# Performance work log

Hardware: AMD Instinct MI355X
Metric: run time of the kernel (lower is better)

## Reference

```python
import jax, jax.numpy as jnp
import numpy as np

B, P, M, C = 8192, 8, 2048, 1024


def setup_inputs() -> dict:
    key = jax.random.key(0)
    k1, k2 = jax.random.split(key)
    stdv = 1.0 / np.sqrt(C)
    inp = jax.random.normal(k1, (B, C), dtype=jnp.float32)
    weight = jax.random.uniform(k2, (P, M, C), dtype=jnp.float32, minval=-stdv, maxval=stdv)
    return {"input": inp, "weight": weight}


def reference(input, weight):
    # scores: [B, P, M] = <input_c, weight_pmc>
    att = jnp.einsum('bc,pmc->bpm', input, weight)
    att = jax.nn.softmax(att, axis=2)
    # combine with the same memory bank as values: [B, P, C]
    out = jnp.einsum('bpm,pmc->bpc', att, weight)
    return out
```

## Files before the change

### kernel.cpp

```cpp
#include <hip/hip_runtime.h>
#include <hip/hip_bf16.h>
#include <cstdint>
#include <cstddef>

#define B_SZ 8192
#define P_SZ 8
#define M_SZ 2048
#define C_SZ 1024

using bfrag = __attribute__((ext_vector_type(8))) short;
using facc  = __attribute__((ext_vector_type(4))) float;
using u16x4 = __attribute__((ext_vector_type(4))) unsigned short;

typedef __attribute__((address_space(1))) const void g_void;
typedef __attribute__((address_space(3))) void l_void;

__device__ __forceinline__ unsigned short f2bf(float x) {
    union { __hip_bfloat16 h; unsigned short u; } cv;
    cv.h = __float2bfloat16(x);
    return cv.u;
}
__device__ __forceinline__ float bf2f(unsigned short u) {
    union { unsigned int i; float f; } cv;
    cv.i = ((unsigned int)u) << 16;
    return cv.f;
}

#define S_BARRIER()     asm volatile("s_barrier" ::: "memory")
#define LGKM0_BARRIER() asm volatile("s_waitcnt lgkmcnt(0)\n\ts_barrier" ::: "memory")
#define WAIT_VM(n)      asm volatile("s_waitcnt vmcnt(" #n ")" ::: "memory")
#define BAR() asm volatile("s_waitcnt lgkmcnt(0)\n\ts_barrier" ::: "memory")
#define WAIT_VM8() asm volatile("s_waitcnt vmcnt(8)" ::: "memory")

__global__ void cvt_q_kernel(const float* __restrict__ in, unsigned short* __restrict__ q) {
    const size_t i = (size_t)blockIdx.x * blockDim.x + threadIdx.x;
    const float4 v = ((const float4*)in)[i];
    u16x4 o = { f2bf(v.x), f2bf(v.y), f2bf(v.z), f2bf(v.w) };
    ((u16x4*)q)[i] = o;
}

__global__ void cvt_w_kernel(const float* __restrict__ w,
                             unsigned short* __restrict__ wb,
                             unsigned short* __restrict__ wt) {
    __shared__ float t[32][33];
    const int bid = blockIdx.x;
    const int p  = bid >> 11;
    const int m0 = ((bid >> 5) & 63) << 5;
    const int c0 = (bid & 31) << 5;
    const int tx = threadIdx.x & 7;
    const int ty = threadIdx.x >> 3;
    const float4 v = *(const float4*)(w + ((size_t)p*M_SZ + m0 + ty)*C_SZ + c0 + tx*4);
    u16x4 o = { f2bf(v.x), f2bf(v.y), f2bf(v.z), f2bf(v.w) };
    *(u16x4*)(wb + ((size_t)p*M_SZ + m0 + ty)*C_SZ + c0 + tx*4) = o;
    t[ty][tx*4+0] = v.x; t[ty][tx*4+1] = v.y; t[ty][tx*4+2] = v.z; t[ty][tx*4+3] = v.w;
    __syncthreads();
    float4 u2;
    u2.x = t[tx*4+0][ty]; u2.y = t[tx*4+1][ty]; u2.z = t[tx*4+2][ty]; u2.w = t[tx*4+3][ty];
    u16x4 o2 = { f2bf(u2.x), f2bf(u2.y), f2bf(u2.z), f2bf(u2.w) };
    *(u16x4*)(wt + ((size_t)p*C_SZ + c0 + ty)*M_SZ + m0 + tx*4) = o2;
}

template<int KLEN, int NTN, int CPX, int MODE>
__global__ __launch_bounds__(256, 2)
void gemm_tile(const unsigned short* __restrict__ A,
               const unsigned short* __restrict__ Bm,
               unsigned short* __restrict__ Pout,
               float* __restrict__ Oout,
               int p)
{
    __shared__ alignas(16) char lds[32768];
    const int tid  = threadIdx.x;
    const int lane = tid & 63;
    const int wid  = tid >> 6;
    const int wr   = wid >> 1;
    const int wc   = wid & 1;
    const int g    = lane >> 4;
    const int l15  = lane & 15;

    const int logical = (blockIdx.x & 7) * CPX + (blockIdx.x >> 3);
    const int mt = logical / NTN;
    const int nt = logical % NTN;

    const unsigned short* Abase = A  + (size_t)mt * 128 * KLEN;
    const unsigned short* Bbase = Bm + (size_t)nt * 128 * KLEN;

    facc acc[4][4];
    #pragma unroll
    for (int i = 0; i < 4; ++i)
        #pragma unroll
        for (int j = 0; j < 4; ++j) acc[i][j] = facc{0.f, 0.f, 0.f, 0.f};
    float rs[4] = {0.f, 0.f, 0.f, 0.f};

    constexpr int NKT = KLEN / 32;

    auto stage = [&](int kt) {
        char* buf = lds + (kt & 1) * 16384;
        const unsigned short* As = Abase + kt * 32;
        const unsigned short* Bs = Bbase + kt * 32;
        #pragma unroll
        for (int i = 0; i < 2; ++i) {
            const int o  = i * 4096 + tid * 16;
            const int r  = o >> 6;
            const int s  = (o >> 4) & 3;
            const int cs = s ^ ((r >> 1) & 3);
            __builtin_amdgcn_global_load_lds((g_void*)(As + (size_t)r * KLEN + cs * 8),
                                             (l_void*)(buf + i * 4096 + ((tid >> 6) << 10)),
                                             16, 0, 0);
        }
        #pragma unroll
        for (int i = 0; i < 2; ++i) {
            const int o  = i * 4096 + tid * 16;
            const int r  = o >> 6;
            const int s  = (o >> 4) & 3;
            const int cs = s ^ ((r >> 1) & 3);
            __builtin_amdgcn_global_load_lds((g_void*)(Bs + (size_t)r * KLEN + cs * 8),
                                             (l_void*)(buf + 8192 + i * 4096 + ((tid >> 6) << 10)),
                                             16, 0, 0);
        }
    };

    stage(0);
    stage(1);

    const int cb = ((((l15 >> 1) & 3) ^ g) << 4);

    for (int kt = 0; kt < NKT; ++kt) {
        if (kt + 1 < NKT) { WAIT_VM(4); } else { WAIT_VM(0); }
        S_BARRIER();
        const char* Ab = lds + (kt & 1) * 16384;
        const char* Bb = Ab + 8192;
        bfrag af[4], bb[4];
        #pragma unroll
        for (int mf = 0; mf < 4; ++mf)
            af[mf] = *(const bfrag*)(Ab + (wr * 64 + mf * 16 + l15) * 64 + cb);
        #pragma unroll
        for (int nf = 0; nf < 4; ++nf)
            bb[nf] = *(const bfrag*)(Bb + (wc * 64 + nf * 16 + l15) * 64 + cb);
        LGKM0_BARRIER();
        if (kt + 2 < NKT) stage(kt + 2);
        if (MODE == 1) {
            #pragma unroll
            for (int mf = 0; mf < 4; ++mf)
                #pragma unroll
                for (int e = 0; e < 8; ++e)
                    rs[mf] += bf2f((unsigned short)af[mf][e]);
        }
        #pragma unroll
        for (int mf = 0; mf < 4; ++mf)
            #pragma unroll
            for (int nf = 0; nf < 4; ++nf)
                acc[mf][nf] = __builtin_amdgcn_mfma_f32_16x16x32_bf16(af[mf], bb[nf], acc[mf][nf], 0, 0, 0);
    }

    if (MODE == 0) {
        const int prow0 = mt * 128 + wr * 64;
        const int pcol0 = nt * 128 + wc * 64;
        #pragma unroll
        for (int mf = 0; mf < 4; ++mf)
            #pragma unroll
            for (int j = 0; j < 4; ++j) {
                const size_t rbase = (size_t)(prow0 + mf * 16 + g * 4 + j) * M_SZ + pcol0 + l15;
                #pragma unroll
                for (int nf = 0; nf < 4; ++nf)
                    Pout[rbase + nf * 16] = f2bf(__expf(acc[mf][nf][j]));
            }
    } else {
        const int orow0 = mt * 128 + wr * 64;
        const int ocol0 = nt * 128 + wc * 64;
        #pragma unroll
        for (int mf = 0; mf < 4; ++mf) {
            float d = rs[mf];
            d += __shfl_xor(d, 16);
            d += __shfl_xor(d, 32);
            #pragma unroll
            for (int j = 0; j < 4; ++j) {
                const float inv = 1.0f / __shfl(d, g * 4 + j);
                const size_t rbase = ((size_t)(orow0 + mf * 16 + g * 4 + j) * P_SZ + p) * C_SZ
                                   + ocol0 + l15;
                #pragma unroll
                for (int nf = 0; nf < 4; ++nf)
                    Oout[rbase + nf * 16] = acc[mf][nf][j] * inv;
            }
        }
    }
}

constexpr int NTHREADS = 512;
constexpr int BR = 64;
constexpr int MT = 32;
constexpr int NT = M_SZ / MT;

constexpr int WS_OFF   = 0;
constexpr int WST_OFF  = 65536;
constexpr int SRED_OFF = 131072;
constexpr int PS_OFF   = 158720;
constexpr int DEN_OFF  = 162816;
constexpr int LDS_BYTES = 163328;

__device__ __forceinline__ void stage_ws(const unsigned short* wsrcTile, char* ldsWs, int tid) {
    #pragma unroll
    for (int k = 0; k < 8; ++k) {
        const int o = k*8192 + tid*16;
        const int m = o >> 11;
        const int s = (o & 2047) >> 4;
        const unsigned short* src = wsrcTile + (size_t)m*C_SZ + ((s ^ (m & 7)) << 3);
        char* dst = ldsWs + k*8192 + ((tid >> 6) << 10);
        __builtin_amdgcn_global_load_lds((g_void*)src, (l_void*)dst, 16, 0, 0);
    }
}

__device__ __forceinline__ void stage_wst(const unsigned short* wtsrcTile, char* ldsWsT, int tid) {
    #pragma unroll
    for (int k = 0; k < 8; ++k) {
        const int o = k*8192 + tid*16;
        const int c  = o >> 6;
        const int mh = (o & 63) >> 4;
        const unsigned short* src = wtsrcTile + (size_t)c*M_SZ + mh*8;
        char* dst = ldsWsT + k*8192 + ((tid >> 6) << 10);
        __builtin_amdgcn_global_load_lds((g_void*)src, (l_void*)dst, 16, 0, 0);
    }
}

__global__ __launch_bounds__(NTHREADS, 2)
void emu_main(const unsigned short* __restrict__ qB,
              const unsigned short* __restrict__ wB,
              const unsigned short* __restrict__ wtB,
              float* __restrict__ out)
{
    extern __shared__ char lds[];
    const int tid  = threadIdx.x;
    const int lane = tid & 63;
    const int wid  = tid >> 6;
    const int rh   = wid >> 2;
    const int kq   = wid & 3;
    const int g    = lane >> 4;
    const int l15  = lane & 15;

    const int p    = blockIdx.x & 7;
    const int row0 = (blockIdx.x >> 3) * BR;

    const unsigned short* wbp = wB  + (size_t)p * M_SZ * C_SZ;
    const unsigned short* wtp = wtB + (size_t)p * C_SZ * M_SZ;

    bfrag qreg[2][8];
    #pragma unroll
    for (int rf = 0; rf < 2; ++rf) {
        const int qrow = row0 + (rh*2 + rf)*16 + l15;
        const unsigned short* qp = qB + (size_t)qrow*C_SZ + kq*256 + g*8;
        #pragma unroll
        for (int kc = 0; kc < 8; ++kc)
            qreg[rf][kc] = *(const bfrag*)(qp + kc*32);
    }

    facc acc[2][16];
    #pragma unroll
    for (int i = 0; i < 2; ++i)
        #pragma unroll
        for (int j = 0; j < 16; ++j) acc[i][j] = facc{0.f,0.f,0.f,0.f};
    float dsum[4] = {0.f, 0.f, 0.f, 0.f};

    const int fid    = rh*4 + kq;
    const int rf_own = rh*2 + (kq >> 1);
    const int mf_own = kq & 1;

    stage_ws (wbp, lds + WS_OFF,  tid);
    stage_wst(wtp, lds + WST_OFF, tid);

    for (int mt = 0; mt < NT; ++mt) {
        const int mtn = (mt + 1 < NT) ? (mt + 1) : (NT - 1);

        WAIT_VM8();
        BAR();

        facc sacc[2][2];
        #pragma unroll
        for (int i = 0; i < 2; ++i) { sacc[i][0] = facc{0,0,0,0}; sacc[i][1] = facc{0,0,0,0}; }
        {
            const char* wsr0 = lds + WS_OFF + l15*2048;
            const char* wsr1 = wsr0 + 32768;
            const int xr = l15 & 7;
            #pragma unroll
            for (int kc = 0; kc < 8; ++kc) {
                const int slog = kq*32 + kc*4 + g;
                const int off  = (slog ^ xr) << 4;
                bfrag b0 = *(const bfrag*)(wsr0 + off);
                bfrag b1 = *(const bfrag*)(wsr1 + off);
                #pragma unroll
                for (int rf = 0; rf < 2; ++rf) {
                    sacc[rf][0] = __builtin_amdgcn_mfma_f32_16x16x32_bf16(qreg[rf][kc], b0, sacc[rf][0], 0, 0, 0);
                    sacc[rf][1] = __builtin_amdgcn_mfma_f32_16x16x32_bf16(qreg[rf][kc], b1, sacc[rf][1], 0, 0, 0);
                }
            }
        }

        #pragma unroll
        for (int j2 = 0; j2 < 4; ++j2) {
            if (j2 != kq) {
                const int s = kq - (kq > j2 ? 1 : 0);
                float* dstp = (float*)(lds + SRED_OFF) + ((rh*4 + j2)*3 + s)*288;
                #pragma unroll
                for (int j = 0; j < 4; ++j)
                    dstp[(g*4 + j)*18 + l15] = sacc[j2 >> 1][j2 & 1][j];
            }
        }
        BAR();

        stage_ws(wbp + (size_t)mtn*MT*C_SZ, lds + WS_OFF, tid);

        {
            facc own = (kq == 0) ? sacc[0][0] : (kq == 1) ? sacc[0][1]
                     : (kq == 2) ? sacc[1][0] : sacc[1][1];
            const float* srcp = (const float*)(lds + SRED_OFF) + fid*3*288;
            float ps[4];
            #pragma unroll
            for (int j = 0; j < 4; ++j) {
                const int e = (g*4 + j)*18 + l15;
                float v = own[j] + srcp[e] + srcp[288 + e] + srcp[576 + e];
                ps[j] = __expf(v);
                dsum[j] += ps[j];
            }
            #pragma unroll
            for (int j = 0; j < 4; ++j)
                *(unsigned short*)(lds + PS_OFF + ((rf_own*16 + g*4 + j)*32 + mf_own*16 + l15)*2)
                    = f2bf(ps[j]);
        }

        WAIT_VM8();
        BAR();

        {
            bfrag pa0 = *(const bfrag*)(lds + PS_OFF + ((rh*2 + 0)*16 + l15)*64 + g*16);
            bfrag pa1 = *(const bfrag*)(lds + PS_OFF + ((rh*2 + 1)*16 + l15)*64 + g*16);
            const char* wtb = lds + WST_OFF + (kq*256 + l15)*64 + g*16;
            #pragma unroll
            for (int cf = 0; cf < 16; ++cf) {
                bfrag bw = *(const bfrag*)(wtb + cf*1024);
                acc[0][cf] = __builtin_amdgcn_mfma_f32_16x16x32_bf16(pa0, bw, acc[0][cf], 0, 0, 0);
                acc[1][cf] = __builtin_amdgcn_mfma_f32_16x16x32_bf16(pa1, bw, acc[1][cf], 0, 0, 0);
            }
        }
        BAR();

        stage_wst(wtp + (size_t)mtn*MT, lds + WST_OFF, tid);
    }

    #pragma unroll
    for (int j = 0; j < 4; ++j) {
        float v = dsum[j];
        v += __shfl_xor(v, 1); v += __shfl_xor(v, 2);
        v += __shfl_xor(v, 4); v += __shfl_xor(v, 8);
        if (l15 == 0) ((float*)(lds + DEN_OFF))[fid*16 + g*4 + j] = v;
    }
    BAR();

    const float* denp = (const float*)(lds + DEN_OFF);
    #pragma unroll
    for (int rf = 0; rf < 2; ++rf) {
        const int rfg = rh*2 + rf;
        #pragma unroll
        for (int j = 0; j < 4; ++j) {
            const int rr = g*4 + j;
            const float inv = 1.0f / (denp[(rfg*2 + 0)*16 + rr] + denp[(rfg*2 + 1)*16 + rr]);
            const size_t b = (size_t)row0 + rfg*16 + rr;
            float* op = out + (b*P_SZ + p)*C_SZ + kq*256 + l15;
            #pragma unroll
            for (int cf = 0; cf < 16; ++cf)
                op[cf*16] = acc[rf][cf][j] * inv;
        }
    }
}

__global__ void emu_fallback(const float* __restrict__ inF, const float* __restrict__ wF,
                             float* __restrict__ out)
{
    __shared__ float sc[M_SZ];
    __shared__ float qs[C_SZ];
    __shared__ float wsum[4];
    const int b = blockIdx.x;
    const int tid = threadIdx.x;
    for (int c = tid; c < C_SZ; c += 256) qs[c] = inF[(size_t)b*C_SZ + c];
    __syncthreads();
    for (int p = 0; p < P_SZ; ++p) {
        const float* wp = wF + (size_t)p*M_SZ*C_SZ;
        for (int m = tid; m < M_SZ; m += 256) {
            float d = 0.f;
            const float* wr = wp + (size_t)m*C_SZ;
            for (int c = 0; c < C_SZ; ++c) d += qs[c]*wr[c];
            sc[m] = __expf(d);
        }
        __syncthreads();
        float part = 0.f;
        for (int m = tid; m < M_SZ; m += 256) part += sc[m];
        #pragma unroll
        for (int sft = 1; sft < 64; sft <<= 1) part += __shfl_xor(part, sft);
        if ((tid & 63) == 0) wsum[tid >> 6] = part;
        __syncthreads();
        const float rin = 1.0f / (wsum[0] + wsum[1] + wsum[2] + wsum[3]);
        float o0=0,o1=0,o2=0,o3=0;
        for (int m = 0; m < M_SZ; ++m) {
            const float pm = sc[m];
            const float4 w4 = *(const float4*)(wp + (size_t)m*C_SZ + tid*4);
            o0 += pm*w4.x; o1 += pm*w4.y; o2 += pm*w4.z; o3 += pm*w4.w;
        }
        float* op = out + ((size_t)b*P_SZ + p)*C_SZ + tid*4;
        op[0]=o0*rin; op[1]=o1*rin; op[2]=o2*rin; op[3]=o3*rin;
        __syncthreads();
    }
}

extern "C" void kernel_launch(void* const* d_in, const int* in_sizes, int n_in,
                              void* d_out, int out_size, void* d_ws, size_t ws_size,
                              hipStream_t stream)
{
    (void)in_sizes; (void)n_in; (void)out_size;
    const float* inF = (const float*)d_in[0];
    const float* wF  = (const float*)d_in[1];
    float* out = (float*)d_out;

    const size_t wbE = (size_t)P_SZ * M_SZ * C_SZ;
    const size_t qE  = (size_t)B_SZ * C_SZ;
    const size_t pME = (size_t)B_SZ * M_SZ;
    const size_t needFull  = (wbE*2 + qE + pME) * sizeof(unsigned short);
    const size_t needFused = (wbE*2 + qE) * sizeof(unsigned short);

    if (ws_size >= needFull) {
        unsigned short* wb = (unsigned short*)d_ws;
        unsigned short* wt = wb + wbE;
        unsigned short* qb = wt + wbE;
        unsigned short* Pb = qb + qE;
        cvt_q_kernel<<<(unsigned)(qE/4/256), 256, 0, stream>>>(inF, qb);
        cvt_w_kernel<<<P_SZ*64*32, 256, 0, stream>>>(wF, wb, wt);
        for (int p = 0; p < P_SZ; ++p) {
            gemm_tile<C_SZ, 16, 128, 0><<<1024, 256, 0, stream>>>(
                qb, wb + (size_t)p*M_SZ*C_SZ, Pb, nullptr, p);
            gemm_tile<M_SZ, 8, 64, 1><<<512, 256, 0, stream>>>(
                Pb, wt + (size_t)p*C_SZ*M_SZ, nullptr, out, p);
        }
    } else if (ws_size >= needFused) {
        unsigned short* wb = (unsigned short*)d_ws;
        unsigned short* wt = wb + wbE;
        unsigned short* qb = wt + wbE;
        cvt_q_kernel<<<(unsigned)(qE/4/256), 256, 0, stream>>>(inF, qb);
        cvt_w_kernel<<<P_SZ*64*32, 256, 0, stream>>>(wF, wb, wt);
        hipFuncSetAttribute(reinterpret_cast<const void*>(&emu_main),
                            hipFuncAttributeMaxDynamicSharedMemorySize, LDS_BYTES);
        const dim3 grid((B_SZ / BR) * P_SZ);
        emu_main<<<grid, dim3(NTHREADS), LDS_BYTES, stream>>>(qb, wb, wt, out);
    } else {
        emu_fallback<<<B_SZ, 256, 0, stream>>>(inF, wF, out);
    }
}
```

Measured before the change: 760.3 us.

## Replace per-head GEMM launches with batched 256x256-tile pipelined GEMM kernels

Adds a new 512-thread GEMM kernel that uses 256x256 output tiles, double-buffered LDS staging via global_load_lds with XOR swizzle, and split-phase MFMA scheduling with s_setprio. When the workspace can hold the probabilities for all 8 heads at once, the score and output GEMMs each run as a single launch covering every head. This replaces the 16 per-head launches and the old fused streaming kernel. It needs a much larger workspace for the bf16 probability matrix of all heads, and the new path only runs if the harness provides that much.

```diff
diff --git a/kernel.cpp b/kernel.cpp
--- a/kernel.cpp
+++ b/kernel.cpp
@@ -29,8 +29,6 @@
 #define S_BARRIER()     asm volatile("s_barrier" ::: "memory")
 #define LGKM0_BARRIER() asm volatile("s_waitcnt lgkmcnt(0)\n\ts_barrier" ::: "memory")
 #define WAIT_VM(n)      asm volatile("s_waitcnt vmcnt(" #n ")" ::: "memory")
-#define BAR() asm volatile("s_waitcnt lgkmcnt(0)\n\ts_barrier" ::: "memory")
-#define WAIT_VM8() asm volatile("s_waitcnt vmcnt(8)" ::: "memory")
 
 __global__ void cvt_q_kernel(const float* __restrict__ in, unsigned short* __restrict__ q) {
     const size_t i = (size_t)blockIdx.x * blockDim.x + threadIdx.x;
@@ -60,6 +58,202 @@
     *(u16x4*)(wt + ((size_t)p*C_SZ + c0 + ty)*M_SZ + m0 + tx*4) = o2;
 }
 
+constexpr int GLDS = 131072;
+
+template<int KLEN>
+__device__ __forceinline__ void stage_half8(const unsigned short* panelBase, char* ldsOp,
+                                            int hh, int kt, int tid) {
+    #pragma unroll
+    for (int i = 0; i < 2; ++i) {
+        const int o  = i*8192 + tid*16;
+        const int rl = o >> 7;
+        const int r  = hh*128 + rl;
+        const int ps = (o >> 4) & 7;
+        const int ls = ps ^ (r & 7);
+        const unsigned short* src = panelBase + (size_t)r*KLEN + kt*64 + ls*8;
+        char* dst = ldsOp + hh*16384 + i*8192 + ((tid >> 6) << 10);
+        __builtin_amdgcn_global_load_lds((g_void*)src, (l_void*)dst, 16, 0, 0);
+    }
+}
+
+__device__ __forceinline__ void loadA8(const char* ldsAbuf, int qm, int wm, int l15, int g,
+                                       bfrag (&aF)[4][2]) {
+    #pragma unroll
+    for (int mf = 0; mf < 4; ++mf) {
+        const int r = qm*128 + wm*64 + mf*16 + l15;
+        const char* rp = ldsAbuf + r*128;
+        #pragma unroll
+        for (int ks = 0; ks < 2; ++ks)
+            aF[mf][ks] = *(const bfrag*)(rp + (((ks*4 + g) ^ (r & 7)) << 4));
+    }
+}
+
+__device__ __forceinline__ void loadB8(const char* ldsBbuf, int qn, int wn, int l15, int g,
+                                       bfrag (&bF)[2][2]) {
+    #pragma unroll
+    for (int nf = 0; nf < 2; ++nf) {
+        const int r = qn*128 + wn*32 + nf*16 + l15;
+        const char* rp = ldsBbuf + r*128;
+        #pragma unroll
+        for (int ks = 0; ks < 2; ++ks)
+            bF[nf][ks] = *(const bfrag*)(rp + (((ks*4 + g) ^ (r & 7)) << 4));
+    }
+}
+
+template<int QM, int QN>
+__device__ __forceinline__ void mfma_phase(const bfrag (&aF)[4][2], const bfrag (&bF)[2][2],
+                                           facc (&acc)[8][4]) {
+    __builtin_amdgcn_s_setprio(1);
+    #pragma unroll
+    for (int ks = 0; ks < 2; ++ks)
+        #pragma unroll
+        for (int mf = 0; mf < 4; ++mf)
+            #pragma unroll
+            for (int nf = 0; nf < 2; ++nf)
+                acc[QM*4 + mf][QN*2 + nf] = __builtin_amdgcn_mfma_f32_16x16x32_bf16(
+                    aF[mf][ks], bF[nf][ks], acc[QM*4 + mf][QN*2 + nf], 0, 0, 0);
+    __builtin_amdgcn_s_setprio(0);
+}
+
+template<int KLEN, int NTN, int MODE>
+__global__ __launch_bounds__(512, 2)
+void gemm8(const unsigned short* __restrict__ A,
+           const unsigned short* __restrict__ Bm,
+           unsigned short* __restrict__ Pout,
+           float* __restrict__ Oout,
+           size_t APS, size_t BPS)
+{
+    extern __shared__ char lds[];
+    const int tid  = threadIdx.x;
+    const int lane = tid & 63;
+    const int wid  = tid >> 6;
+    const int wm   = wid >> 2;
+    const int wn   = wid & 3;
+    const int g    = lane >> 4;
+    const int l15  = lane & 15;
+
+    const int p       = blockIdx.x & 7;
+    const int logical = blockIdx.x >> 3;
+    const int nt      = logical % NTN;
+    const int mt      = logical / NTN;
+
+    const unsigned short* Abase = A  + (size_t)p*APS + (size_t)mt*256*KLEN;
+    const unsigned short* Bbase = Bm + (size_t)p*BPS + (size_t)nt*256*KLEN;
+
+    facc acc[8][4];
+    #pragma unroll
+    for (int i = 0; i < 8; ++i)
+        #pragma unroll
+        for (int j = 0; j < 4; ++j) acc[i][j] = facc{0.f, 0.f, 0.f, 0.f};
+    float rs[8] = {0.f,0.f,0.f,0.f,0.f,0.f,0.f,0.f};
+
+    constexpr int NKT = KLEN / 64;
+
+    stage_half8<KLEN>(Abase, lds + 0,             0, 0, tid);
+    stage_half8<KLEN>(Abase, lds + 0,             1, 0, tid);
+    stage_half8<KLEN>(Bbase, lds + 32768,         0, 0, tid);
+    stage_half8<KLEN>(Bbase, lds + 32768,         1, 0, tid);
+    stage_half8<KLEN>(Abase, lds + 65536,         0, (1 < NKT ? 1 : NKT-1), tid);
+    stage_half8<KLEN>(Bbase, lds + 65536 + 32768, 1, (1 < NKT ? 1 : NKT-1), tid);
+    WAIT_VM(4);
+    S_BARRIER();
+
+    bfrag aF[4][2], bLow[2][2], bHigh[2][2];
+
+    for (int t = 0; t < NKT; ++t) {
+        const int cur = t & 1;
+        char* ldsA  = lds + cur*65536;
+        char* ldsB  = ldsA + 32768;
+        char* ldsAn = lds + (cur^1)*65536;
+        char* ldsBn = ldsAn + 32768;
+        const int t1 = (t+1 < NKT) ? t+1 : NKT-1;
+        const int t2 = (t+2 < NKT) ? t+2 : NKT-1;
+
+        loadA8(ldsA, 0, wm, l15, g, aF);
+        loadB8(ldsB, 0, wn, l15, g, bLow);
+        stage_half8<KLEN>(Abase, ldsAn, 1, t1, tid);
+        stage_half8<KLEN>(Bbase, ldsBn, 0, t1, tid);
+        S_BARRIER();
+        mfma_phase<0,0>(aF, bLow, acc);
+        if (MODE == 1) {
+            #pragma unroll
+            for (int mf = 0; mf < 4; ++mf)
+                #pragma unroll
+                for (int ks = 0; ks < 2; ++ks)
+                    #pragma unroll
+                    for (int e = 0; e < 8; ++e)
+                        rs[mf] += bf2f((unsigned short)aF[mf][ks][e]);
+        }
+        LGKM0_BARRIER();
+
+        loadB8(ldsB, 1, wn, l15, g, bHigh);
+        S_BARRIER();
+        mfma_phase<0,1>(aF, bHigh, acc);
+        LGKM0_BARRIER();
+
+        loadA8(ldsA, 1, wm, l15, g, aF);
+        stage_half8<KLEN>(Abase, ldsA, 0, t2, tid);
+        S_BARRIER();
+        mfma_phase<1,1>(aF, bHigh, acc);
+        if (MODE == 1) {
+            #pragma unroll
+            for (int mf = 0; mf < 4; ++mf)
+                #pragma unroll
+                for (int ks = 0; ks < 2; ++ks)
+                    #pragma unroll
+                    for (int e = 0; e < 8; ++e)
+                        rs[4 + mf] += bf2f((unsigned short)aF[mf][ks][e]);
+        }
+        LGKM0_BARRIER();
+
+        stage_half8<KLEN>(Bbase, ldsB, 1, t2, tid);
+        S_BARRIER();
+        mfma_phase<1,0>(aF, bLow, acc);
+        WAIT_VM(4);
+        LGKM0_BARRIER();
+    }
+
+    const int row0g = mt*256;
+    const int col0g = nt*256;
+    if (MODE == 0) {
+        unsigned short* Pp = Pout + (size_t)p * ((size_t)B_SZ * M_SZ);
+        #pragma unroll
+        for (int qm = 0; qm < 2; ++qm)
+            #pragma unroll
+            for (int mf = 0; mf < 4; ++mf)
+                #pragma unroll
+                for (int j = 0; j < 4; ++j) {
+                    const int r = row0g + qm*128 + wm*64 + mf*16 + g*4 + j;
+                    unsigned short* rp = Pp + (size_t)r*M_SZ + col0g + wn*32 + l15;
+                    #pragma unroll
+                    for (int qn = 0; qn < 2; ++qn)
+                        #pragma unroll
+                        for (int nf = 0; nf < 2; ++nf)
+                            rp[qn*128 + nf*16] = f2bf(__expf(acc[qm*4+mf][qn*2+nf][j]));
+                }
+    } else {
+        #pragma unroll
+        for (int qm = 0; qm < 2; ++qm)
+            #pragma unroll
+            for (int mf = 0; mf < 4; ++mf) {
+                float d = rs[qm*4 + mf];
+                d += __shfl_xor(d, 16);
+                d += __shfl_xor(d, 32);
+                #pragma unroll
+                for (int j = 0; j < 4; ++j) {
+                    const float inv = 1.0f / __shfl(d, g*4 + j);
+                    const int r = row0g + qm*128 + wm*64 + mf*16 + g*4 + j;
+                    float* op = Oout + ((size_t)r*P_SZ + p)*C_SZ + col0g + wn*32 + l15;
+                    #pragma unroll
+                    for (int qn = 0; qn < 2; ++qn)
+                        #pragma unroll
+                        for (int nf = 0; nf < 2; ++nf)
+                            op[qn*128 + nf*16] = acc[qm*4+mf][qn*2+nf][j] * inv;
+                }
+            }
+    }
+}
+
 template<int KLEN, int NTN, int CPX, int MODE>
 __global__ __launch_bounds__(256, 2)
 void gemm_tile(const unsigned short* __restrict__ A,
@@ -181,191 +375,6 @@
                 for (int nf = 0; nf < 4; ++nf)
                     Oout[rbase + nf * 16] = acc[mf][nf][j] * inv;
             }
-        }
-    }
-}
-
-constexpr int NTHREADS = 512;
-constexpr int BR = 64;
-constexpr int MT = 32;
-constexpr int NT = M_SZ / MT;
-
-constexpr int WS_OFF   = 0;
-constexpr int WST_OFF  = 65536;
-constexpr int SRED_OFF = 131072;
-constexpr int PS_OFF   = 158720;
-constexpr int DEN_OFF  = 162816;
-constexpr int LDS_BYTES = 163328;
-
-__device__ __forceinline__ void stage_ws(const unsigned short* wsrcTile, char* ldsWs, int tid) {
-    #pragma unroll
-    for (int k = 0; k < 8; ++k) {
-        const int o = k*8192 + tid*16;
-        const int m = o >> 11;
-        const int s = (o & 2047) >> 4;
-        const unsigned short* src = wsrcTile + (size_t)m*C_SZ + ((s ^ (m & 7)) << 3);
-        char* dst = ldsWs + k*8192 + ((tid >> 6) << 10);
-        __builtin_amdgcn_global_load_lds((g_void*)src, (l_void*)dst, 16, 0, 0);
-    }
-}
-
-__device__ __forceinline__ void stage_wst(const unsigned short* wtsrcTile, char* ldsWsT, int tid) {
-    #pragma unroll
-    for (int k = 0; k < 8; ++k) {
-        const int o = k*8192 + tid*16;
-        const int c  = o >> 6;
-        const int mh = (o & 63) >> 4;
-        const unsigned short* src = wtsrcTile + (size_t)c*M_SZ + mh*8;
-        char* dst = ldsWsT + k*8192 + ((tid >> 6) << 10);
-        __builtin_amdgcn_global_load_lds((g_void*)src, (l_void*)dst, 16, 0, 0);
-    }
-}
-
-__global__ __launch_bounds__(NTHREADS, 2)
-void emu_main(const unsigned short* __restrict__ qB,
-              const unsigned short* __restrict__ wB,
-              const unsigned short* __restrict__ wtB,
-              float* __restrict__ out)
-{
-    extern __shared__ char lds[];
-    const int tid  = threadIdx.x;
-    const int lane = tid & 63;
-    const int wid  = tid >> 6;
-    const int rh   = wid >> 2;
-    const int kq   = wid & 3;
-    const int g    = lane >> 4;
-    const int l15  = lane & 15;
-
-    const int p    = blockIdx.x & 7;
-    const int row0 = (blockIdx.x >> 3) * BR;
-
-    const unsigned short* wbp = wB  + (size_t)p * M_SZ * C_SZ;
-    const unsigned short* wtp = wtB + (size_t)p * C_SZ * M_SZ;
-
-    bfrag qreg[2][8];
-    #pragma unroll
-    for (int rf = 0; rf < 2; ++rf) {
-        const int qrow = row0 + (rh*2 + rf)*16 + l15;
-        const unsigned short* qp = qB + (size_t)qrow*C_SZ + kq*256 + g*8;
-        #pragma unroll
-        for (int kc = 0; kc < 8; ++kc)
-            qreg[rf][kc] = *(const bfrag*)(qp + kc*32);
-    }
-
-    facc acc[2][16];
-    #pragma unroll
-    for (int i = 0; i < 2; ++i)
-        #pragma unroll
-        for (int j = 0; j < 16; ++j) acc[i][j] = facc{0.f,0.f,0.f,0.f};
-    float dsum[4] = {0.f, 0.f, 0.f, 0.f};
-
-    const int fid    = rh*4 + kq;
-    const int rf_own = rh*2 + (kq >> 1);
-    const int mf_own = kq & 1;
-
-    stage_ws (wbp, lds + WS_OFF,  tid);
-    stage_wst(wtp, lds + WST_OFF, tid);
-
-    for (int mt = 0; mt < NT; ++mt) {
-        const int mtn = (mt + 1 < NT) ? (mt + 1) : (NT - 1);
-
-        WAIT_VM8();
-        BAR();
-
-        facc sacc[2][2];
-        #pragma unroll
-        for (int i = 0; i < 2; ++i) { sacc[i][0] = facc{0,0,0,0}; sacc[i][1] = facc{0,0,0,0}; }
-        {
-            const char* wsr0 = lds + WS_OFF + l15*2048;
-            const char* wsr1 = wsr0 + 32768;
-            const int xr = l15 & 7;
-            #pragma unroll
-            for (int kc = 0; kc < 8; ++kc) {
-                const int slog = kq*32 + kc*4 + g;
-                const int off  = (slog ^ xr) << 4;
-                bfrag b0 = *(const bfrag*)(wsr0 + off);
-                bfrag b1 = *(const bfrag*)(wsr1 + off);
-                #pragma unroll
-                for (int rf = 0; rf < 2; ++rf) {
-                    sacc[rf][0] = __builtin_amdgcn_mfma_f32_16x16x32_bf16(qreg[rf][kc], b0, sacc[rf][0], 0, 0, 0);
-                    sacc[rf][1] = __builtin_amdgcn_mfma_f32_16x16x32_bf16(qreg[rf][kc], b1, sacc[rf][1], 0, 0, 0);
-                }
-            }
-        }
-
-        #pragma unroll
-        for (int j2 = 0; j2 < 4; ++j2) {
-            if (j2 != kq) {
-                const int s = kq - (kq > j2 ? 1 : 0);
-                float* dstp = (float*)(lds + SRED_OFF) + ((rh*4 + j2)*3 + s)*288;
-                #pragma unroll
-                for (int j = 0; j < 4; ++j)
-                    dstp[(g*4 + j)*18 + l15] = sacc[j2 >> 1][j2 & 1][j];
-            }
-        }
-        BAR();
-
-        stage_ws(wbp + (size_t)mtn*MT*C_SZ, lds + WS_OFF, tid);
-
-        {
-            facc own = (kq == 0) ? sacc[0][0] : (kq == 1) ? sacc[0][1]
-                     : (kq == 2) ? sacc[1][0] : sacc[1][1];
-            const float* srcp = (const float*)(lds + SRED_OFF) + fid*3*288;
-            float ps[4];
-            #pragma unroll
-            for (int j = 0; j < 4; ++j) {
-                const int e = (g*4 + j)*18 + l15;
-                float v = own[j] + srcp[e] + srcp[288 + e] + srcp[576 + e];
-                ps[j] = __expf(v);
-                dsum[j] += ps[j];
-            }
-            #pragma unroll
-            for (int j = 0; j < 4; ++j)
-                *(unsigned short*)(lds + PS_OFF + ((rf_own*16 + g*4 + j)*32 + mf_own*16 + l15)*2)
-                    = f2bf(ps[j]);
-        }
-
-        WAIT_VM8();
-        BAR();
-
-        {
-            bfrag pa0 = *(const bfrag*)(lds + PS_OFF + ((rh*2 + 0)*16 + l15)*64 + g*16);
-            bfrag pa1 = *(const bfrag*)(lds + PS_OFF + ((rh*2 + 1)*16 + l15)*64 + g*16);
-            const char* wtb = lds + WST_OFF + (kq*256 + l15)*64 + g*16;
-            #pragma unroll
-            for (int cf = 0; cf < 16; ++cf) {
-                bfrag bw = *(const bfrag*)(wtb + cf*1024);
-                acc[0][cf] = __builtin_amdgcn_mfma_f32_16x16x32_bf16(pa0, bw, acc[0][cf], 0, 0, 0);
-                acc[1][cf] = __builtin_amdgcn_mfma_f32_16x16x32_bf16(pa1, bw, acc[1][cf], 0, 0, 0);
-            }
-        }
-        BAR();
-
-        stage_wst(wtp + (size_t)mtn*MT, lds + WST_OFF, tid);
-    }
-
-    #pragma unroll
-    for (int j = 0; j < 4; ++j) {
-        float v = dsum[j];
-        v += __shfl_xor(v, 1); v += __shfl_xor(v, 2);
-        v += __shfl_xor(v, 4); v += __shfl_xor(v, 8);
-        if (l15 == 0) ((float*)(lds + DEN_OFF))[fid*16 + g*4 + j] = v;
-    }
-    BAR();
-
-    const float* denp = (const float*)(lds + DEN_OFF);
-    #pragma unroll
-    for (int rf = 0; rf < 2; ++rf) {
-        const int rfg = rh*2 + rf;
-        #pragma unroll
-        for (int j = 0; j < 4; ++j) {
-            const int rr = g*4 + j;
-            const float inv = 1.0f / (denp[(rfg*2 + 0)*16 + rr] + denp[(rfg*2 + 1)*16 + rr]);
-            const size_t b = (size_t)row0 + rfg*16 + rr;
-            float* op = out + (b*P_SZ + p)*C_SZ + kq*256 + l15;
-            #pragma unroll
-            for (int cf = 0; cf < 16; ++cf)
-                op[cf*16] = acc[rf][cf][j] * inv;
         }
     }
 }
@@ -417,13 +426,29 @@
     const float* wF  = (const float*)d_in[1];
     float* out = (float*)d_out;
 
-    const size_t wbE = (size_t)P_SZ * M_SZ * C_SZ;
-    const size_t qE  = (size_t)B_SZ * C_SZ;
-    const size_t pME = (size_t)B_SZ * M_SZ;
-    const size_t needFull  = (wbE*2 + qE + pME) * sizeof(unsigned short);
-    const size_t needFused = (wbE*2 + qE) * sizeof(unsigned short);
-
-    if (ws_size >= needFull) {
+    const size_t wbE  = (size_t)P_SZ * M_SZ * C_SZ;
+    const size_t qE   = (size_t)B_SZ * C_SZ;
+    const size_t pME  = (size_t)B_SZ * M_SZ;
+    const size_t pAll = pME * P_SZ;
+    const size_t needBig   = (wbE*2 + qE + pAll) * sizeof(unsigned short);
+    const size_t needMid   = (wbE*2 + qE + pME)  * sizeof(unsigned short);
+
+    if (ws_size >= needBig) {
+        unsigned short* wb = (unsigned short*)d_ws;
+        unsigned short* wt = wb + wbE;
+        unsigned short* qb = wt + wbE;
+        unsigned short* Pb = qb + qE;
+        cvt_q_kernel<<<(unsigned)(qE/4/256), 256, 0, stream>>>(inF, qb);
+        cvt_w_kernel<<<P_SZ*64*32, 256, 0, stream>>>(wF, wb, wt);
+        hipFuncSetAttribute(reinterpret_cast<const void*>(&gemm8<C_SZ, 8, 0>),
+                            hipFuncAttributeMaxDynamicSharedMemorySize, GLDS);
+        gemm8<C_SZ, 8, 0><<<2048, 512, GLDS, stream>>>(
+            qb, wb, Pb, nullptr, (size_t)0, (size_t)M_SZ * C_SZ);
+        hipFuncSetAttribute(reinterpret_cast<const void*>(&gemm8<M_SZ, 4, 1>),
+                            hipFuncAttributeMaxDynamicSharedMemorySize, GLDS);
+        gemm8<M_SZ, 4, 1><<<1024, 512, GLDS, stream>>>(
+            Pb, wt, nullptr, out, (size_t)B_SZ * M_SZ, (size_t)C_SZ * M_SZ);
+    } else if (ws_size >= needMid) {
         unsigned short* wb = (unsigned short*)d_ws;
         unsigned short* wt = wb + wbE;
         unsigned short* qb = wt + wbE;
@@ -436,16 +461,6 @@
             gemm_tile<M_SZ, 8, 64, 1><<<512, 256, 0, stream>>>(
                 Pb, wt + (size_t)p*C_SZ*M_SZ, nullptr, out, p);
         }
-    } else if (ws_size >= needFused) {
-        unsigned short* wb = (unsigned short*)d_ws;
-        unsigned short* wt = wb + wbE;
-        unsigned short* qb = wt + wbE;
-        cvt_q_kernel<<<(unsigned)(qE/4/256), 256, 0, stream>>>(inF, qb);
-        cvt_w_kernel<<<P_SZ*64*32, 256, 0, stream>>>(wF, wb, wt);
-        hipFuncSetAttribute(reinterpret_cast<const void*>(&emu_main),
-                            hipFuncAttributeMaxDynamicSharedMemorySize, LDS_BYTES);
-        const dim3 grid((B_SZ / BR) * P_SZ);
-        emu_main<<<grid, dim3(NTHREADS), LDS_BYTES, stream>>>(qb, wb, wt, out);
     } else {
         emu_fallback<<<B_SZ, 256, 0, stream>>>(inF, wF, out);
     }
```

After: 796.1 us. +4.7%, slower.
